# Performance work log

Measured on AMD Instinct MI355X. Metric: run time of the kernel, lower is better.

## Reference

```python
import jax, jax.numpy as jnp
import numpy as np
import math

L, S, N, E, H = 2048, 2048, 2, 512, 8
D = E // H


def setup_inputs() -> dict:
    key = jax.random.key(0)
    ks = jax.random.split(key, 12)
    scale = 1.0 / math.sqrt(E)
    return {
        "query": jax.random.normal(ks[0], (L, N, E), jnp.float32),
        "key": jax.random.normal(ks[1], (S, N, E), jnp.float32),
        "value": jax.random.normal(ks[2], (S, N, E), jnp.float32),
        "attn_bias": jax.random.normal(ks[3], (L, S), jnp.float32),
        "Wq": jax.random.normal(ks[4], (E, E), jnp.float32) * scale,
        "bq": jnp.zeros((E,), jnp.float32),
        "Wk": jax.random.normal(ks[5], (E, E), jnp.float32) * scale,
        "bk": jnp.zeros((E,), jnp.float32),
        "Wv": jax.random.normal(ks[6], (E, E), jnp.float32) * scale,
        "bv": jnp.zeros((E,), jnp.float32),
        "Wo": jax.random.normal(ks[7], (E, E), jnp.float32) * scale,
        "bo": jnp.zeros((E,), jnp.float32),
    }


def reference(query, key, value, attn_bias, Wq, bq, Wk, bk, Wv, bv, Wo, bo):
    # Linear projections (nn.Linear: x @ W.T + b)
    Q = (query @ Wq.T + bq).reshape(L, N, H, D)
    K = (key @ Wk.T + bk).reshape(S, N, H, D)
    V = (value @ Wv.T + bv).reshape(S, N, H, D)
    # scores: [H, N, L, S]
    scores = jnp.einsum("lnhd,snhd->hnls", Q, K) / math.sqrt(D)
    scores = scores + attn_bias[None, None, :, :]
    attn_weights = jax.nn.softmax(scores, axis=-1)  # dropout p=0 / eval
    # attention output: [L, N, H, D] -> [L, N, E]
    attn_out = jnp.einsum("hnls,snhd->lnhd", attn_weights, V).reshape(L, N, E)
    attn_out = attn_out @ Wo.T + bo
    return attn_out, attn_weights.reshape(H * N, L, S)
```

## Files before the change

### kernel.cpp

```cpp
#include <hip/hip_runtime.h>
#include <hip/hip_bf16.h>
#include <math.h>

#define L_SEQ 2048
#define S_SEQ 2048
#define N_B 2
#define E_DIM 512
#define H_HEADS 8
#define D_HEAD 64
#define M_ROWS (L_SEQ * N_B)
#define BH (H_HEADS * N_B)

typedef __attribute__((ext_vector_type(8))) short bf16x8;
typedef __attribute__((ext_vector_type(4))) float f32x4;

#define MFMA(a, b, c) __builtin_amdgcn_mfma_f32_16x16x32_bf16((a), (b), (c), 0, 0, 0)

__device__ __forceinline__ short f2bf(float v) {
    union { __hip_bfloat16 h; short s; } u;
    u.h = __float2bfloat16(v);
    return u.s;
}
__device__ __forceinline__ float bf2f(short s) {
    union { __hip_bfloat16 h; short t; } u;
    u.t = s;
    return __bfloat162float(u.h);
}
__device__ __forceinline__ void cvt8_hl(const float4& a, const float4& b, bf16x8& h, bf16x8& l) {
    float v[8] = {a.x, a.y, a.z, a.w, b.x, b.y, b.z, b.w};
#pragma unroll
    for (int i = 0; i < 8; ++i) {
        short hh = f2bf(v[i]);
        h[i] = hh;
        l[i] = f2bf(v[i] - bf2f(hh));
    }
}
__device__ __forceinline__ bf16x8 cvt8_h(const float4& a, const float4& b) {
    float v[8] = {a.x, a.y, a.z, a.w, b.x, b.y, b.z, b.w};
    bf16x8 h;
#pragma unroll
    for (int i = 0; i < 8; ++i) h[i] = f2bf(v[i]);
    return h;
}

__global__ __launch_bounds__(256) void fill_kernel(float4* __restrict__ p, int n4) {
    const float4 z = {0.f, 0.f, 0.f, 0.f};
    for (int i = blockIdx.x * 256 + threadIdx.x; i < n4; i += gridDim.x * 256) p[i] = z;
}

__global__ __launch_bounds__(256) void proj_qkv_kernel(
    const float* __restrict__ X, const float* __restrict__ W,
    const float* __restrict__ bias, short* __restrict__ outH, short* __restrict__ outL) {
    __shared__ __align__(16) short Ah[64 * 40], Al[64 * 40], Bh[64 * 40], Bl[64 * 40];
    const int bn = blockIdx.x * 64;
    const int bm = blockIdx.y * 64;
    const int tid = threadIdx.x;
    const int wave = tid >> 6, lane = tid & 63;
    const int m16 = lane & 15, q = lane >> 4;
    const int srow = tid >> 2, sk = (tid & 3) * 8;

    f32x4 acc[4] = {};

    for (int k0 = 0; k0 < E_DIM; k0 += 32) {
        {
            const float4* pa = (const float4*)(X + (size_t)(bm + srow) * E_DIM + k0 + sk);
            float4 a0 = pa[0], a1 = pa[1];
            const float4* pb = (const float4*)(W + (size_t)(bn + srow) * E_DIM + k0 + sk);
            float4 b0 = pb[0], b1 = pb[1];
            bf16x8 vh, vl;
            cvt8_hl(a0, a1, vh, vl);
            *(bf16x8*)&Ah[srow * 40 + sk] = vh;
            *(bf16x8*)&Al[srow * 40 + sk] = vl;
            cvt8_hl(b0, b1, vh, vl);
            *(bf16x8*)&Bh[srow * 40 + sk] = vh;
            *(bf16x8*)&Bl[srow * 40 + sk] = vl;
        }
        __syncthreads();
        const bf16x8 ah = *(const bf16x8*)&Ah[(wave * 16 + m16) * 40 + q * 8];
        const bf16x8 al = *(const bf16x8*)&Al[(wave * 16 + m16) * 40 + q * 8];
#pragma unroll
        for (int j = 0; j < 4; ++j) {
            const bf16x8 bh_ = *(const bf16x8*)&Bh[(j * 16 + m16) * 40 + q * 8];
            const bf16x8 bl_ = *(const bf16x8*)&Bl[(j * 16 + m16) * 40 + q * 8];
            acc[j] = MFMA(ah, bh_, acc[j]);
            acc[j] = MFMA(ah, bl_, acc[j]);
            acc[j] = MFMA(al, bh_, acc[j]);
        }
        __syncthreads();
    }

#pragma unroll
    for (int j = 0; j < 4; ++j) {
        const int e = bn + j * 16 + m16;
        const int h = e >> 6, d = e & 63;
        const float be = bias[e];
#pragma unroll
        for (int r = 0; r < 4; ++r) {
            const int row = bm + wave * 16 + q * 4 + r;
            const int l = row >> 1, n = row & 1;
            const float v = acc[j][r] + be;
            const size_t idx = ((size_t)(h * 2 + n) * L_SEQ + l) * D_HEAD + d;
            const short hi = f2bf(v);
            outH[idx] = hi;
            outL[idx] = f2bf(v - bf2f(hi));
        }
    }
}

__global__ __launch_bounds__(256) void vtrans_kernel(const short* __restrict__ Vb,
                                                     short* __restrict__ Vt) {
    __shared__ short tile[64][65];
    const int s0 = blockIdx.x * 64;
    const int bh = blockIdx.y;
    const int t = threadIdx.x;
    const int r = t >> 2, seg = (t & 3) * 16;
    const bf16x8* p = (const bf16x8*)(Vb + ((size_t)bh * S_SEQ + s0 + r) * D_HEAD + seg);
    bf16x8 v0 = p[0], v1 = p[1];
#pragma unroll
    for (int i = 0; i < 8; ++i) {
        tile[r][seg + i] = v0[i];
        tile[r][seg + 8 + i] = v1[i];
    }
    __syncthreads();
    bf16x8 o0, o1;
#pragma unroll
    for (int i = 0; i < 8; ++i) {
        o0[i] = tile[seg + i][r];
        o1[i] = tile[seg + 8 + i][r];
    }
    bf16x8* po = (bf16x8*)(Vt + ((size_t)bh * D_HEAD + r) * S_SEQ + s0 + seg);
    po[0] = o0;
    po[1] = o1;
}

__global__ __launch_bounds__(512) void scores_pv_kernel(
    const short* __restrict__ Qh, const short* __restrict__ Ql,
    const short* __restrict__ Kh, const short* __restrict__ Kl,
    const short* __restrict__ Vt, const float* __restrict__ bias,
    float* __restrict__ wout, short* __restrict__ ctx) {
    const int bh = blockIdx.y;
    const int l0 = blockIdx.x * 16;
    const int tid = threadIdx.x;
    const int wave = tid >> 6, lane = tid & 63;
    const int m16 = lane & 15, q = lane >> 4;
    const int sbase = wave * 256;

    __shared__ float LMAX[8][16], LSUM[8][16];
    __shared__ __align__(16) float SM_T[8][32][17];
    __shared__ __align__(16) float OB[8][16][65];

    const size_t qoff = ((size_t)bh * L_SEQ + l0 + m16) * D_HEAD;
    bf16x8 aH[2], aL[2];
#pragma unroll
    for (int ks = 0; ks < 2; ++ks) {
        aH[ks] = *(const bf16x8*)(Qh + qoff + ks * 32 + q * 8);
        aL[ks] = *(const bf16x8*)(Ql + qoff + ks * 32 + q * 8);
    }

    f32x4 C[16] = {};
#pragma unroll
    for (int t = 0; t < 16; ++t) {
        const size_t koff = ((size_t)bh * S_SEQ + sbase + t * 16 + m16) * D_HEAD;
#pragma unroll
        for (int ks = 0; ks < 2; ++ks) {
            const bf16x8 kh = *(const bf16x8*)(Kh + koff + ks * 32 + q * 8);
            const bf16x8 kl = *(const bf16x8*)(Kl + koff + ks * 32 + q * 8);
            C[t] = MFMA(aH[ks], kh, C[t]);
            C[t] = MFMA(aH[ks], kl, C[t]);
            C[t] = MFMA(aL[ks], kh, C[t]);
        }
    }

    const int row0 = l0 + q * 4;
#pragma unroll
    for (int r = 0; r < 4; ++r) {
        const float* brow = bias + (size_t)(row0 + r) * S_SEQ + sbase + m16;
#pragma unroll
        for (int t = 0; t < 16; ++t) C[t][r] = C[t][r] * 0.125f + brow[t * 16];
    }

    float mx[4] = {-INFINITY, -INFINITY, -INFINITY, -INFINITY};
#pragma unroll
    for (int t = 0; t < 16; ++t)
#pragma unroll
        for (int r = 0; r < 4; ++r) mx[r] = fmaxf(mx[r], C[t][r]);
#pragma unroll
    for (int d = 1; d < 16; d <<= 1)
#pragma unroll
        for (int r = 0; r < 4; ++r) mx[r] = fmaxf(mx[r], __shfl_xor(mx[r], d, 64));
    if (m16 == 0) {
#pragma unroll
        for (int r = 0; r < 4; ++r) LMAX[wave][q * 4 + r] = mx[r];
    }
    __syncthreads();
    float M[4];
#pragma unroll
    for (int r = 0; r < 4; ++r) {
        float v = -INFINITY;
#pragma unroll
        for (int w = 0; w < 8; ++w) v = fmaxf(v, LMAX[w][q * 4 + r]);
        M[r] = v;
    }

    float sm[4] = {};
#pragma unroll
    for (int t = 0; t < 16; ++t)
#pragma unroll
        for (int r = 0; r < 4; ++r) {
            const float e = __expf(C[t][r] - M[r]);
            C[t][r] = e;
            sm[r] += e;
        }
#pragma unroll
    for (int d = 1; d < 16; d <<= 1)
#pragma unroll
        for (int r = 0; r < 4; ++r) sm[r] += __shfl_xor(sm[r], d, 64);
    if (m16 == 0) {
#pragma unroll
        for (int r = 0; r < 4; ++r) LSUM[wave][q * 4 + r] = sm[r];
    }
    __syncthreads();
#pragma unroll
    for (int r = 0; r < 4; ++r) {
        float s = 0.f;
#pragma unroll
        for (int w = 0; w < 8; ++w) s += LSUM[w][q * 4 + r];
        const float inv = 1.0f / s;
        float* orow = wout + ((size_t)bh * L_SEQ + row0 + r) * S_SEQ + sbase + m16;
#pragma unroll
        for (int t = 0; t < 16; ++t) {
            C[t][r] *= inv;
            orow[t * 16] = C[t][r];
        }
    }

    f32x4 O[4] = {};
    float (*T)[17] = SM_T[wave];
    for (int c = 0; c < 8; ++c) {
        __syncthreads();
#pragma unroll
        for (int r = 0; r < 4; ++r) {
            T[m16][q * 4 + r]      = C[2 * c][r];
            T[16 + m16][q * 4 + r] = C[2 * c + 1][r];
        }
        __syncthreads();
        bf16x8 a;
#pragma unroll
        for (int j = 0; j < 8; ++j) a[j] = f2bf(T[q * 8 + j][m16]);
        const int scol = sbase + c * 32;
#pragma unroll
        for (int j = 0; j < 4; ++j) {
            const bf16x8 b =
                *(const bf16x8*)(Vt + ((size_t)bh * D_HEAD + j * 16 + m16) * S_SEQ + scol + q * 8);
            O[j] = MFMA(a, b, O[j]);
        }
    }

    __syncthreads();
#pragma unroll
    for (int j = 0; j < 4; ++j)
#pragma unroll
        for (int r = 0; r < 4; ++r) OB[wave][q * 4 + r][j * 16 + m16] = O[j][r];
    __syncthreads();

    const int h = bh >> 1, n = bh & 1;
#pragma unroll
    for (int u = 0; u < 2; ++u) {
        const int idx = tid + u * 512;
        const int row = idx >> 6, d = idx & 63;
        float s = 0.f;
#pragma unroll
        for (int w = 0; w < 8; ++w) s += OB[w][row][d];
        ctx[(size_t)((l0 + row) * N_B + n) * E_DIM + h * D_HEAD + d] = f2bf(s);
    }
}

__global__ __launch_bounds__(256) void oproj_kernel(const short* __restrict__ ctx,
                                                    const float* __restrict__ W,
                                                    const float* __restrict__ bias,
                                                    float* __restrict__ out) {
    __shared__ __align__(16) short Bh[64 * 40];
    const int bn = blockIdx.x * 64;
    const int bm = blockIdx.y * 64;
    const int tid = threadIdx.x;
    const int wave = tid >> 6, lane = tid & 63;
    const int m16 = lane & 15, q = lane >> 4;
    const int srow = tid >> 2, sk = (tid & 3) * 8;

    f32x4 acc[4] = {};
    for (int k0 = 0; k0 < E_DIM; k0 += 32) {
        {
            const float4* pb = (const float4*)(W + (size_t)(bn + srow) * E_DIM + k0 + sk);
            *(bf16x8*)&Bh[srow * 40 + sk] = cvt8_h(pb[0], pb[1]);
        }
        __syncthreads();
        const bf16x8 a = *(const bf16x8*)(ctx + (size_t)(bm + wave * 16 + m16) * E_DIM + k0 + q * 8);
#pragma unroll
        for (int j = 0; j < 4; ++j) {
            const bf16x8 b = *(const bf16x8*)&Bh[(j * 16 + m16) * 40 + q * 8];
            acc[j] = MFMA(a, b, acc[j]);
        }
        __syncthreads();
    }
#pragma unroll
    for (int j = 0; j < 4; ++j) {
        const int e = bn + j * 16 + m16;
        const float be = bias[e];
#pragma unroll
        for (int r = 0; r < 4; ++r)
            out[(size_t)(bm + wave * 16 + q * 4 + r) * E_DIM + e] = acc[j][r] + be;
    }
}

extern "C" void kernel_launch(void* const* d_in, const int* in_sizes, int n_in,
                              void* d_out, int out_size, void* d_ws, size_t ws_size,
                              hipStream_t stream) {
    const float* query = (const float*)d_in[0];
    const float* key   = (const float*)d_in[1];
    const float* value = (const float*)d_in[2];
    const float* bias  = (const float*)d_in[3];
    const float* Wq    = (const float*)d_in[4];
    const float* bq    = (const float*)d_in[5];
    const float* Wk    = (const float*)d_in[6];
    const float* bk    = (const float*)d_in[7];
    const float* Wv    = (const float*)d_in[8];
    const float* bv    = (const float*)d_in[9];
    const float* Wo    = (const float*)d_in[10];
    const float* bo    = (const float*)d_in[11];

    float* out0 = (float*)d_out;
    float* wgt  = out0 + (size_t)M_ROWS * E_DIM;

    short* wsS = (short*)d_ws;
    const size_t buf = (size_t)BH * L_SEQ * D_HEAD;
    short* Qh  = wsS + 0 * buf;
    short* Ql  = wsS + 1 * buf;
    short* Kh  = wsS + 2 * buf;
    short* Kl  = wsS + 3 * buf;
    short* Vh  = wsS + 4 * buf;
    short* Vt  = wsS + 5 * buf;
    short* ctx = wsS + 6 * buf;

    fill_kernel<<<2048, 256, 0, stream>>>((float4*)d_ws, (int)(7 * buf * sizeof(short) / 16));

    const dim3 gproj(E_DIM / 64, M_ROWS / 64);
    proj_qkv_kernel<<<gproj, 256, 0, stream>>>(query, Wq, bq, Qh, Ql);
    proj_qkv_kernel<<<gproj, 256, 0, stream>>>(key, Wk, bk, Kh, Kl);
    proj_qkv_kernel<<<gproj, 256, 0, stream>>>(value, Wv, bv, Vh, ctx);

    vtrans_kernel<<<dim3(S_SEQ / 64, BH), 256, 0, stream>>>(Vh, Vt);

    scores_pv_kernel<<<dim3(L_SEQ / 16, BH), 512, 0, stream>>>(Qh, Ql, Kh, Kl, Vt, bias, wgt, ctx);

    oproj_kernel<<<gproj, 256, 0, stream>>>(ctx, Wo, bo, out0);
}
```

Before: 572.9 us.

## Pre-split inputs and weights to bf16 hi/lo and drop LDS staging in projections

Adds a split kernel that converts the fp32 activations and weights to bf16 hi/lo pairs once, into scratch regions borrowed from the workspace and from the tail of the attention-weights output. The projection kernel then reads MFMA operands directly from global memory with no LDS staging and no barriers. This removes the fp32-to-bf16 conversion from the GEMM inner loop, which was repeated per tile. The V projection also skips writing its unused low half. The cost is six extra kernel launches, extra global traffic, and uncoalesced, unshared per-wave global loads, with weight reads duplicated across waves.

```diff
diff --git a/kernel.cpp b/kernel.cpp
--- a/kernel.cpp
+++ b/kernel.cpp
@@ -48,45 +48,45 @@
     for (int i = blockIdx.x * 256 + threadIdx.x; i < n4; i += gridDim.x * 256) p[i] = z;
 }
 
-__global__ __launch_bounds__(256) void proj_qkv_kernel(
-    const float* __restrict__ X, const float* __restrict__ W,
-    const float* __restrict__ bias, short* __restrict__ outH, short* __restrict__ outL) {
-    __shared__ __align__(16) short Ah[64 * 40], Al[64 * 40], Bh[64 * 40], Bl[64 * 40];
+__global__ __launch_bounds__(256) void split_kernel(const float* __restrict__ in,
+                                                    short* __restrict__ hi,
+                                                    short* __restrict__ lo, int n8) {
+    const int i = blockIdx.x * 256 + threadIdx.x;
+    if (i >= n8) return;
+    const float4* p = (const float4*)(in + (size_t)i * 8);
+    bf16x8 h, l;
+    cvt8_hl(p[0], p[1], h, l);
+    *(bf16x8*)(hi + (size_t)i * 8) = h;
+    *(bf16x8*)(lo + (size_t)i * 8) = l;
+}
+
+__global__ __launch_bounds__(256) void proj_kernel(
+    const short* __restrict__ Xh, const short* __restrict__ Xl,
+    const short* __restrict__ Wh, const short* __restrict__ Wl,
+    const float* __restrict__ bias, short* __restrict__ outH,
+    short* __restrict__ outL, int writeLo) {
     const int bn = blockIdx.x * 64;
     const int bm = blockIdx.y * 64;
     const int tid = threadIdx.x;
     const int wave = tid >> 6, lane = tid & 63;
     const int m16 = lane & 15, q = lane >> 4;
-    const int srow = tid >> 2, sk = (tid & 3) * 8;
+
+    const short* pAh = Xh + (size_t)(bm + wave * 16 + m16) * E_DIM;
+    const short* pAl = Xl + (size_t)(bm + wave * 16 + m16) * E_DIM;
 
     f32x4 acc[4] = {};
-
     for (int k0 = 0; k0 < E_DIM; k0 += 32) {
-        {
-            const float4* pa = (const float4*)(X + (size_t)(bm + srow) * E_DIM + k0 + sk);
-            float4 a0 = pa[0], a1 = pa[1];
-            const float4* pb = (const float4*)(W + (size_t)(bn + srow) * E_DIM + k0 + sk);
-            float4 b0 = pb[0], b1 = pb[1];
-            bf16x8 vh, vl;
-            cvt8_hl(a0, a1, vh, vl);
-            *(bf16x8*)&Ah[srow * 40 + sk] = vh;
-            *(bf16x8*)&Al[srow * 40 + sk] = vl;
-            cvt8_hl(b0, b1, vh, vl);
-            *(bf16x8*)&Bh[srow * 40 + sk] = vh;
-            *(bf16x8*)&Bl[srow * 40 + sk] = vl;
-        }
-        __syncthreads();
-        const bf16x8 ah = *(const bf16x8*)&Ah[(wave * 16 + m16) * 40 + q * 8];
-        const bf16x8 al = *(const bf16x8*)&Al[(wave * 16 + m16) * 40 + q * 8];
+        const bf16x8 ah = *(const bf16x8*)(pAh + k0 + q * 8);
+        const bf16x8 al = *(const bf16x8*)(pAl + k0 + q * 8);
 #pragma unroll
         for (int j = 0; j < 4; ++j) {
-            const bf16x8 bh_ = *(const bf16x8*)&Bh[(j * 16 + m16) * 40 + q * 8];
-            const bf16x8 bl_ = *(const bf16x8*)&Bl[(j * 16 + m16) * 40 + q * 8];
+            const size_t bo = (size_t)(bn + j * 16 + m16) * E_DIM + k0 + q * 8;
+            const bf16x8 bh_ = *(const bf16x8*)(Wh + bo);
+            const bf16x8 bl_ = *(const bf16x8*)(Wl + bo);
             acc[j] = MFMA(ah, bh_, acc[j]);
             acc[j] = MFMA(ah, bl_, acc[j]);
             acc[j] = MFMA(al, bh_, acc[j]);
         }
-        __syncthreads();
     }
 
 #pragma unroll
@@ -97,12 +97,12 @@
 #pragma unroll
         for (int r = 0; r < 4; ++r) {
             const int row = bm + wave * 16 + q * 4 + r;
-            const int l = row >> 1, n = row & 1;
+            const int l = row >> 1, nb = row & 1;
             const float v = acc[j][r] + be;
-            const size_t idx = ((size_t)(h * 2 + n) * L_SEQ + l) * D_HEAD + d;
+            const size_t idx = ((size_t)(h * 2 + nb) * L_SEQ + l) * D_HEAD + d;
             const short hi = f2bf(v);
             outH[idx] = hi;
-            outL[idx] = f2bf(v - bf2f(hi));
+            if (writeLo) outL[idx] = f2bf(v - bf2f(hi));
         }
     }
 }
@@ -338,15 +338,29 @@
     short* Kh  = wsS + 2 * buf;
     short* Kl  = wsS + 3 * buf;
     short* Vh  = wsS + 4 * buf;
-    short* Vt  = wsS + 5 * buf;
-    short* ctx = wsS + 6 * buf;
+    short* Vt  = wsS + 5 * buf;   short* Xl = Vt;
+    short* ctx = wsS + 6 * buf;   short* Xh = ctx;
+
+    const size_t wb = (size_t)E_DIM * E_DIM;
+    const size_t wgtElems = (size_t)BH * L_SEQ * S_SEQ;
+    short* WhT = (short*)wgt + 2 * wgtElems - 2 * wb;
+    short* WlT = WhT + wb;
+
+    const int nW8 = (int)(wb / 8);
+    const int nX8 = (int)((size_t)M_ROWS * E_DIM / 8);
+    const dim3 gproj(E_DIM / 64, M_ROWS / 64);
 
     fill_kernel<<<2048, 256, 0, stream>>>((float4*)d_ws, (int)(7 * buf * sizeof(short) / 16));
 
-    const dim3 gproj(E_DIM / 64, M_ROWS / 64);
-    proj_qkv_kernel<<<gproj, 256, 0, stream>>>(query, Wq, bq, Qh, Ql);
-    proj_qkv_kernel<<<gproj, 256, 0, stream>>>(key, Wk, bk, Kh, Kl);
-    proj_qkv_kernel<<<gproj, 256, 0, stream>>>(value, Wv, bv, Vh, ctx);
+    split_kernel<<<nX8 / 256, 256, 0, stream>>>(query, Xh, Xl, nX8);
+    split_kernel<<<nW8 / 256, 256, 0, stream>>>(Wq, WhT, WlT, nW8);
+    proj_kernel<<<gproj, 256, 0, stream>>>(Xh, Xl, WhT, WlT, bq, Qh, Ql, 1);
+    split_kernel<<<nX8 / 256, 256, 0, stream>>>(key, Xh, Xl, nX8);
+    split_kernel<<<nW8 / 256, 256, 0, stream>>>(Wk, WhT, WlT, nW8);
+    proj_kernel<<<gproj, 256, 0, stream>>>(Xh, Xl, WhT, WlT, bk, Kh, Kl, 1);
+    split_kernel<<<nX8 / 256, 256, 0, stream>>>(value, Xh, Xl, nX8);
+    split_kernel<<<nW8 / 256, 256, 0, stream>>>(Wv, WhT, WlT, nW8);
+    proj_kernel<<<gproj, 256, 0, stream>>>(Xh, Xl, WhT, WlT, bv, Vh, (short*)wgt, 0);
 
     vtrans_kernel<<<dim3(S_SEQ / 64, BH), 256, 0, stream>>>(Vh, Vt);
 
```

After: 652.7 us. 1.14x slower.
